# Optimization experiments

Hardware: AMD Instinct MI355X
Metric: run time of the kernel (lower is better)

## Reference

```python
import jax, jax.numpy as jnp
import numpy as np

N_QUBITS = 10
N_LATENT = 6
N_LAYERS = 2
AMP_DIM = 2 ** N_QUBITS  # 1024


def _apply_1q(state, gate, q):
    # state: [B] + [2]*N_QUBITS complex; gate: [2,2]; wire q -> axis q+1 (wire 0 = MSB)
    s = jnp.tensordot(gate, state, axes=[[1], [q + 1]])  # new axis at front
    return jnp.moveaxis(s, 0, q + 1)


def _ry_mat(theta):
    c = jnp.cos(theta / 2)
    s = jnp.sin(theta / 2)
    return jnp.stack([jnp.stack([c, -s]), jnp.stack([s, c])]).astype(jnp.complex64)


def _rz_mat(theta):
    half = theta / 2
    e = jnp.cos(half) + 1j * jnp.sin(half)  # e^{i theta/2}
    zero = jnp.zeros((), jnp.complex64)
    return jnp.stack([jnp.stack([jnp.conj(e), zero]), jnp.stack([zero, e])]).astype(jnp.complex64)


def _cnot(state, c, t):
    # flip target axis where control bit == 1
    ctrl_shape = [1] * (N_QUBITS + 1)
    ctrl_shape[c + 1] = 2
    ctrl = jnp.arange(2).reshape(ctrl_shape)
    return jnp.where(ctrl == 1, jnp.flip(state, axis=t + 1), state)


def _expvals(state):
    # PauliX, PauliY, PauliZ on wires 0..N_LATENT-1  -> [B, 3*N_LATENT]
    rest = tuple(range(1, N_QUBITS))  # axes of the 9 remaining wires after a take
    xs, ys, zs = [], [], []
    for q in range(N_LATENT):
        s0 = jnp.take(state, 0, axis=q + 1)
        s1 = jnp.take(state, 1, axis=q + 1)
        z01 = jnp.conj(s0) * s1
        xs.append(2.0 * jnp.sum(z01.real, axis=rest))
        ys.append(2.0 * jnp.sum(z01.imag, axis=rest))
        zs.append(jnp.sum(jnp.abs(s0) ** 2 - jnp.abs(s1) ** 2, axis=rest))
    return jnp.stack(xs + ys + zs, axis=1)


def _simulate(x, weights):
    B, D = x.shape
    if D < AMP_DIM:
        x = jnp.pad(x, ((0, 0), (0, AMP_DIM - D)))
    else:
        x = x[:, :AMP_DIM]
    norm = jnp.maximum(jnp.linalg.norm(x, axis=-1, keepdims=True), 1e-8)
    x = x / norm
    state = x.astype(jnp.complex64).reshape((B,) + (2,) * N_QUBITS)
    for layer in range(N_LAYERS):
        off = layer * N_QUBITS * 3
        for q in range(N_QUBITS):
            state = _apply_1q(state, _ry_mat(weights[off + q]), q)
        for q in range(N_QUBITS):
            state = _apply_1q(state, _rz_mat(weights[off + N_QUBITS + q]), q)
        for q in range(N_QUBITS):
            state = _cnot(state, q, (q + 1) % N_QUBITS)
        for q in range(N_QUBITS):
            state = _apply_1q(state, _ry_mat(weights[off + 2 * N_QUBITS + q]), q)
    return _expvals(state).astype(jnp.float32)


def setup_inputs() -> dict:
    key = jax.random.key(0)
    k1, k2 = jax.random.split(key)
    B, D = 32768, 768
    x = jax.random.normal(k1, (B, D), dtype=jnp.float32)
    std = np.sqrt(2.0 / (N_QUBITS + N_LAYERS)).astype(np.float32)
    weights = jax.random.normal(k2, (N_LAYERS * N_QUBITS * 3,), dtype=jnp.float32) * std
    return {"x": x, "weights": weights}


def reference(x, weights):
    return _simulate(x, weights)
```

## Files before the change

kernel.cpp:

```cpp
#include <hip/hip_runtime.h>

#define DIN 768

typedef float f2 __attribute__((ext_vector_type(2)));
typedef int i2v __attribute__((ext_vector_type(2)));

#if __has_builtin(__builtin_amdgcn_permlane32_swap)
#define HAVE_PL32 1
#endif
#if __has_builtin(__builtin_amdgcn_permlane16_swap)
#define HAVE_PL16 1
#endif

__device__ __forceinline__ int f2i(float v) { return __builtin_bit_cast(int, v); }
__device__ __forceinline__ float i2f(int v) { return __builtin_bit_cast(float, v); }

template<int CTRL>
__device__ __forceinline__ float dppf(float v) {
  const int i = f2i(v);
  return i2f(__builtin_amdgcn_update_dpp(i, i, CTRL, 0xF, 0xF, true));
}
template<int CTRL>
__device__ __forceinline__ f2 dppf2(f2 v) {
  f2 r; r.x = dppf<CTRL>(v.x); r.y = dppf<CTRL>(v.y); return r;
}

__device__ __forceinline__ f2 wsum2(f2 v) {
  v += dppf2<0xB1>(v);
  v += dppf2<0x4E>(v);
  v += dppf2<0x124>(v);
  v += dppf2<0x128>(v);
#ifdef HAVE_PL16
  { i2v rx = __builtin_amdgcn_permlane16_swap(f2i(v.x), f2i(v.x), false, false);
    i2v ry = __builtin_amdgcn_permlane16_swap(f2i(v.y), f2i(v.y), false, false);
    v.x = i2f(rx.x) + i2f(rx.y);
    v.y = i2f(ry.x) + i2f(ry.y); }
#else
  v.x += __shfl_xor(v.x, 16); v.y += __shfl_xor(v.y, 16);
#endif
#ifdef HAVE_PL32
  { i2v rx = __builtin_amdgcn_permlane32_swap(f2i(v.x), f2i(v.x), false, false);
    i2v ry = __builtin_amdgcn_permlane32_swap(f2i(v.y), f2i(v.y), false, false);
    v.x = i2f(rx.x) + i2f(rx.y);
    v.y = i2f(ry.x) + i2f(ry.y); }
#else
  v.x += __shfl_xor(v.x, 32); v.y += __shfl_xor(v.y, 32);
#endif
  return v;
}

template<int MASK>
__device__ __forceinline__ f2 shflx_f2(f2 v, int lane) {
  f2 r;
  if constexpr (MASK == 1) {
    r = dppf2<0xB1>(v);
  } else if constexpr (MASK == 2) {
    r = dppf2<0x4E>(v);
  } else if constexpr (MASK == 4) {
    r.x = i2f(__builtin_amdgcn_ds_swizzle(f2i(v.x), 0x101F));
    r.y = i2f(__builtin_amdgcn_ds_swizzle(f2i(v.y), 0x101F));
  } else if constexpr (MASK == 8) {
    r = dppf2<0x128>(v);
  } else if constexpr (MASK == 16) {
#ifdef HAVE_PL16
    const i2v a = __builtin_amdgcn_permlane16_swap(f2i(v.x), f2i(v.x), false, false);
    const i2v b = __builtin_amdgcn_permlane16_swap(f2i(v.y), f2i(v.y), false, false);
    const bool hi = (lane >> 4) & 1;
    r.x = hi ? i2f(a.x) : i2f(a.y);
    r.y = hi ? i2f(b.x) : i2f(b.y);
#else
    r.x = __shfl_xor(v.x, 16); r.y = __shfl_xor(v.y, 16);
#endif
  } else if constexpr (MASK == 32) {
#ifdef HAVE_PL32
    const i2v a = __builtin_amdgcn_permlane32_swap(f2i(v.x), f2i(v.x), false, false);
    const i2v b = __builtin_amdgcn_permlane32_swap(f2i(v.y), f2i(v.y), false, false);
    const bool lo = lane < 32;
    r.x = lo ? i2f(a.y) : i2f(a.x);
    r.y = lo ? i2f(b.y) : i2f(b.x);
#else
    r.x = __shfl_xor(v.x, 32); r.y = __shfl_xor(v.y, 32);
#endif
  } else {
    r.x = __shfl_xor(v.x, MASK); r.y = __shfl_xor(v.y, MASK);
  }
  return r;
}

__device__ __forceinline__ int swzf(int i) { return i ^ ((i >> 4) & 31); }

__device__ __forceinline__ int cnotL(int i) {
  const int b9 = (i >> 9) & 1;
  const int b8 = (i >> 8) & 1;
  const int b0 = i & 1;
  return ((i ^ (i >> 1)) & 0xFF) | ((b8 ^ b9 ^ b0) << 8) | ((b9 ^ b0) << 9);
}

template<int RB>
__device__ __forceinline__ void ry1(f2 (&a)[16], float c, float s) {
#pragma unroll
  for (int r = 0; r < 16; ++r) {
    if (!(r & (1 << RB))) {
      const int p = r | (1 << RB);
      const f2 a0 = a[r], a1 = a[p];
      a[r] = a0 * c - a1 * s;
      a[p] = a1 * c + a0 * s;
    }
  }
}
template<int RB>
__device__ __forceinline__ void ry2(f2 (&re)[16], f2 (&im)[16], float c, float s) {
  ry1<RB>(re, c, s);
  ry1<RB>(im, c, s);
}
template<int MASK>
__device__ __forceinline__ void ry1_shfl(int lane, f2 (&a)[16], float c, float s) {
  const float ss = (lane & MASK) ? s : -s;
#pragma unroll
  for (int r = 0; r < 16; ++r) {
    const f2 p = shflx_f2<MASK>(a[r], lane);
    a[r] = a[r] * c + p * ss;
  }
}

template<int RB>
__device__ __forceinline__ void xyr(const f2 (&re)[16], const f2 (&im)[16], f2& aX, f2& aY) {
#pragma unroll
  for (int r = 0; r < 16; ++r) {
    if (!(r & (1 << RB))) {
      const int p = r | (1 << RB);
      aX += re[r] * re[p] + im[r] * im[p];
      aY += re[r] * im[p] - im[r] * re[p];
    }
  }
}
template<int MASK>
__device__ __forceinline__ void xys(int lane, const f2 (&re)[16], const f2 (&im)[16], f2& aX, f2& aY) {
  const float sgn = (lane & MASK) ? -1.f : 1.f;
#pragma unroll
  for (int r = 0; r < 16; ++r) {
    const f2 pr = shflx_f2<MASK>(re[r], lane);
    const f2 pi = shflx_f2<MASK>(im[r], lane);
    aX += re[r] * pr + im[r] * pi;
    aY += (re[r] * pi - im[r] * pr) * sgn;
  }
}

__global__ void qae_prep(const float* __restrict__ w, float2* __restrict__ ws) {
  const int i = threadIdx.x;
  if (i < 50) {
    float s, c; __sincosf(0.5f * w[i], &s, &c);
    ws[i] = make_float2(c, s);
  } else if (i < 56) {
    float s, c; __sincosf(w[i], &s, &c);
    ws[i] = make_float2(c, s);
  } else if (i < 60) {
    ws[i] = make_float2(1.f, 0.f);
  } else if (i < 70) {
    const int q = i - 60;
    float s, c; __sincosf(0.5f * (w[20 + q] + w[30 + q]), &s, &c);
    ws[i] = make_float2(c, s);
  }
  if (i < 16) {
    float p1 = 0.f, p2 = 0.f;
#pragma unroll
    for (int k = 0; k < 4; ++k) {
      const float sg = ((i >> k) & 1) ? 0.5f : -0.5f;
      p1 += sg * w[10 + 3 - k];
      p2 += sg * w[40 + 3 - k];
    }
    float s, c;
    __sincosf(p1, &s, &c); ws[70 + i] = make_float2(c, s);
    __sincosf(p2, &s, &c); ws[86 + i] = make_float2(c, s);
  }
  if (i < 64) {
    float p1 = 0.f, p2 = 0.f;
#pragma unroll
    for (int b = 0; b < 6; ++b) {
      const float sg = ((i >> b) & 1) ? 0.5f : -0.5f;
      p1 += sg * w[10 + 9 - b];
      p2 += sg * w[40 + 9 - b];
    }
    float s, c;
    __sincosf(p1, &s, &c); ws[102 + i] = make_float2(c, s);
    __sincosf(p2, &s, &c); ws[166 + i] = make_float2(c, s);
  }
}

#define STC8(boff) (*reinterpret_cast<f2*>(reinterpret_cast<char*>(stc) + (boff)))

__global__ __launch_bounds__(64) void qae_main(const float* __restrict__ x,
                                               const float2* __restrict__ gt,
                                               float* __restrict__ out, int Btot) {
  __shared__ f2 stc[1024];
  const int lane = threadIdx.x;
  const int b0   = blockIdx.x * 2, b1 = b0 + 1;
  const bool has1 = (b1 < Btot);

  const float2 L1 = gt[102 + lane];
  const float2 L2 = gt[166 + lane];

  const int bA8   = swzf(lane << 4) << 3;
  const int sL8   = swzf(lane) << 3;
  const int bCA8  = swzf(cnotL(lane << 4)) << 3;
  const int bCB8  = swzf(cnotL(lane)) << 3;

  f2 g[16];
  f2 ss = (f2){0.f, 0.f};
  const float* x0 = x + (size_t)b0 * DIN;
  const float* x1 = x + (size_t)b1 * DIN;
#pragma unroll
  for (int r = 0; r < 12; ++r) {
    const int i = (r << 6) | lane;
    const float va = x0[i];
    const float vb = has1 ? x1[i] : 0.f;
    g[r] = (f2){va, vb};
    ss += g[r] * g[r];
  }
#pragma unroll
  for (int r = 12; r < 16; ++r) g[r] = (f2){0.f, 0.f};
  ss = wsum2(ss);
  const f2 inv = (f2){1.f / fmaxf(ss.x, 1e-16f), 1.f / fmaxf(ss.y, 1e-16f)};

  float2 cs;
  cs = gt[0]; ry1<3>(g, cs.x, cs.y);
  cs = gt[1]; ry1<2>(g, cs.x, cs.y);
  cs = gt[2]; ry1<1>(g, cs.x, cs.y);
  cs = gt[3]; ry1<0>(g, cs.x, cs.y);
  cs = gt[4]; ry1_shfl<32>(lane, g, cs.x, cs.y);
  cs = gt[5]; ry1_shfl<16>(lane, g, cs.x, cs.y);
  cs = gt[6]; ry1_shfl<8>(lane, g, cs.x, cs.y);
  cs = gt[7]; ry1_shfl<4>(lane, g, cs.x, cs.y);
  cs = gt[8]; ry1_shfl<2>(lane, g, cs.x, cs.y);
  cs = gt[9]; ry1_shfl<1>(lane, g, cs.x, cs.y);

  f2 re[16], im[16];
#pragma unroll
  for (int r = 0; r < 16; ++r) {
    const float2 R = gt[70 + r];
    const float kre = R.x * L1.x - R.y * L1.y;
    const float kim = R.x * L1.y + R.y * L1.x;
    re[r] = g[r] * kre;
    im[r] = g[r] * kim;
  }

#pragma unroll
  for (int r = 0; r < 16; ++r) STC8((swzf(r << 6) << 3) ^ sL8) = re[r];
#pragma unroll
  for (int r = 0; r < 16; ++r) re[r] = STC8(bCA8 ^ (swzf(cnotL(r)) << 3));
#pragma unroll
  for (int r = 0; r < 16; ++r) STC8((swzf(r << 6) << 3) ^ sL8) = im[r];
#pragma unroll
  for (int r = 0; r < 16; ++r) im[r] = STC8(bCA8 ^ (swzf(cnotL(r)) << 3));

  cs = gt[66]; ry2<3>(re, im, cs.x, cs.y);
  cs = gt[67]; ry2<2>(re, im, cs.x, cs.y);
  cs = gt[68]; ry2<1>(re, im, cs.x, cs.y);
  cs = gt[69]; ry2<0>(re, im, cs.x, cs.y);
  cs = gt[64]; ry1_shfl<2>(lane, re, cs.x, cs.y); ry1_shfl<2>(lane, im, cs.x, cs.y);
  cs = gt[65]; ry1_shfl<1>(lane, re, cs.x, cs.y); ry1_shfl<1>(lane, im, cs.x, cs.y);

#pragma unroll
  for (int r = 0; r < 16; ++r) STC8(bA8 ^ (r << 3)) = re[r];
#pragma unroll
  for (int r = 0; r < 16; ++r) re[r] = STC8((swzf(r << 6) << 3) ^ sL8);
#pragma unroll
  for (int r = 0; r < 16; ++r) STC8(bA8 ^ (r << 3)) = im[r];
#pragma unroll
  for (int r = 0; r < 16; ++r) im[r] = STC8((swzf(r << 6) << 3) ^ sL8);

  cs = gt[60]; ry2<3>(re, im, cs.x, cs.y);
  cs = gt[61]; ry2<2>(re, im, cs.x, cs.y);
  cs = gt[62]; ry2<1>(re, im, cs.x, cs.y);
  cs = gt[63]; ry2<0>(re, im, cs.x, cs.y);

#pragma unroll
  for (int r = 0; r < 16; ++r) {
    const float2 R = gt[86 + r];
    const float kre = R.x * L2.x - R.y * L2.y;
    const float kim = R.x * L2.y + R.y * L2.x;
    const f2 nre = re[r] * kre - im[r] * kim;
    im[r] = re[r] * kim + im[r] * kre;
    re[r] = nre;
  }

#pragma unroll
  for (int r = 0; r < 16; ++r) STC8((swzf(r << 6) << 3) ^ sL8) = re[r];
#pragma unroll
  for (int r = 0; r < 16; ++r) re[r] = STC8(bCB8 ^ (swzf(cnotL(r << 6)) << 3));
#pragma unroll
  for (int r = 0; r < 16; ++r) STC8((swzf(r << 6) << 3) ^ sL8) = im[r];
#pragma unroll
  for (int r = 0; r < 16; ++r) im[r] = STC8(bCB8 ^ (swzf(cnotL(r << 6)) << 3));

  f2 a18[18];
#pragma unroll
  for (int k = 0; k < 12; ++k) a18[k] = (f2){0.f, 0.f};

  {
    f2 psum = (f2){0.f, 0.f};
    f2 z0 = (f2){0.f,0.f}, z1 = (f2){0.f,0.f}, z2 = (f2){0.f,0.f}, z3 = (f2){0.f,0.f};
#pragma unroll
    for (int r = 0; r < 16; ++r) {
      const f2 p = re[r] * re[r] + im[r] * im[r];
      psum += p;
      z0 += (r & 8) ? -p : p;
      z1 += (r & 4) ? -p : p;
      z2 += (r & 2) ? -p : p;
      z3 += (r & 1) ? -p : p;
    }
    a18[12] = z0; a18[13] = z1; a18[14] = z2; a18[15] = z3;
    a18[16] = ((lane >> 5) & 1) ? -psum : psum;
    a18[17] = ((lane >> 4) & 1) ? -psum : psum;
  }

  xyr<3>(re, im, a18[0], a18[6]);
  xyr<2>(re, im, a18[1], a18[7]);
  xyr<1>(re, im, a18[2], a18[8]);
  xyr<0>(re, im, a18[3], a18[9]);
  xys<32>(lane, re, im, a18[4], a18[10]);
  xys<16>(lane, re, im, a18[5], a18[11]);

#pragma unroll
  for (int k = 0; k < 18; ++k) {
    f2 v = a18[k];
    v += dppf2<0xB1>(v);
    v += dppf2<0x4E>(v);
    a18[k] = v;
  }
  float* red = reinterpret_cast<float*>(stc);
  if ((lane & 3) == 0) {
    const int q = lane >> 2;
    f2* redf2 = reinterpret_cast<f2*>(red);
#pragma unroll
    for (int k = 0; k < 18; ++k) redf2[q * 20 + k] = a18[k];
  }
  if (lane < 36) {
    const int c  = (lane >= 18) ? 1 : 0;
    const int j  = lane - 18 * c;
    const int jq = (j < 6) ? j : ((j < 12) ? j - 6 : j - 12);
    const int jp = (j < 6) ? (j + 12) : ((j >= 12) ? (j - 12) : j);
    float S = 0.f, P = 0.f;
#pragma unroll
    for (int q = 0; q < 16; ++q) {
      S += red[(q * 20 + j ) * 2 + c];
      P += red[(q * 20 + jp) * 2 + c];
    }
    const float fac  = (jq < 4) ? 2.f : 1.f;
    const float2 fa  = gt[50 + jq];
    const float invc = c ? inv.y : inv.x;
    float o;
    if (j < 6)       o = (fac * S * fa.x + P * fa.y) * invc;
    else if (j < 12) o = fac * S * invc;
    else             o = (S * fa.x - fac * P * fa.y) * invc;
    if (c == 0 || has1) out[(size_t)(b0 + c) * 18 + j] = o;
  }
}

extern "C" void kernel_launch(void* const* d_in, const int* in_sizes, int n_in,
                              void* d_out, int out_size, void* d_ws, size_t ws_size,
                              hipStream_t stream) {
  const float* x = (const float*)d_in[0];
  const float* w = (const float*)d_in[1];
  float* out = (float*)d_out;
  float2* ws = (float2*)d_ws;
  const int B = in_sizes[0] / DIN;
  qae_prep<<<dim3(1), dim3(1024), 0, stream>>>(w, ws);
  const int grid = (B + 1) / 2;
  qae_main<<<dim3(grid), dim3(64), 0, stream>>>(x, (const float2*)ws, out, B);
}
```

Baseline: 102.9 us.

## Load input with float4 in lane-contiguous layout and transpose via LDS

Input rows are now loaded as float4 with each lane owning 16 contiguous amplitudes, so the low six qubits are in registers and only two need cross-lane shuffles. After applying those gates, the state is transposed through shared memory into the original lane-strided layout for the remaining four RY gates. This replaces four expensive cross-lane shuffles (masks 4, 8, 16, 32) with an extra LDS round trip. It also changes coalescing: per-lane 16-byte loads instead of scalar strided loads.

```diff
diff --git a/kernel.cpp b/kernel.cpp
--- a/kernel.cpp
+++ b/kernel.cpp
@@ -56,11 +56,6 @@
     r = dppf2<0xB1>(v);
   } else if constexpr (MASK == 2) {
     r = dppf2<0x4E>(v);
-  } else if constexpr (MASK == 4) {
-    r.x = i2f(__builtin_amdgcn_ds_swizzle(f2i(v.x), 0x101F));
-    r.y = i2f(__builtin_amdgcn_ds_swizzle(f2i(v.y), 0x101F));
-  } else if constexpr (MASK == 8) {
-    r = dppf2<0x128>(v);
   } else if constexpr (MASK == 16) {
 #ifdef HAVE_PL16
     const i2v a = __builtin_amdgcn_permlane16_swap(f2i(v.x), f2i(v.x), false, false);
@@ -210,29 +205,39 @@
   const float* x0 = x + (size_t)b0 * DIN;
   const float* x1 = x + (size_t)b1 * DIN;
 #pragma unroll
-  for (int r = 0; r < 12; ++r) {
-    const int i = (r << 6) | lane;
-    const float va = x0[i];
-    const float vb = has1 ? x1[i] : 0.f;
-    g[r] = (f2){va, vb};
-    ss += g[r] * g[r];
-  }
-#pragma unroll
-  for (int r = 12; r < 16; ++r) g[r] = (f2){0.f, 0.f};
+  for (int t = 0; t < 4; ++t) {
+    const int idx = lane * 16 + 4 * t;
+    float4 va = make_float4(0.f, 0.f, 0.f, 0.f);
+    float4 vb = make_float4(0.f, 0.f, 0.f, 0.f);
+    if (idx < DIN) {
+      va = *reinterpret_cast<const float4*>(x0 + idx);
+      if (has1) vb = *reinterpret_cast<const float4*>(x1 + idx);
+    }
+    g[4*t+0] = (f2){va.x, vb.x}; g[4*t+1] = (f2){va.y, vb.y};
+    g[4*t+2] = (f2){va.z, vb.z}; g[4*t+3] = (f2){va.w, vb.w};
+#pragma unroll
+    for (int k = 0; k < 4; ++k) ss += g[4*t+k] * g[4*t+k];
+  }
   ss = wsum2(ss);
   const f2 inv = (f2){1.f / fmaxf(ss.x, 1e-16f), 1.f / fmaxf(ss.y, 1e-16f)};
 
   float2 cs;
+  cs = gt[6]; ry1<3>(g, cs.x, cs.y);
+  cs = gt[7]; ry1<2>(g, cs.x, cs.y);
+  cs = gt[8]; ry1<1>(g, cs.x, cs.y);
+  cs = gt[9]; ry1<0>(g, cs.x, cs.y);
+  cs = gt[4]; ry1_shfl<2>(lane, g, cs.x, cs.y);
+  cs = gt[5]; ry1_shfl<1>(lane, g, cs.x, cs.y);
+
+#pragma unroll
+  for (int r = 0; r < 16; ++r) STC8(bA8 ^ (r << 3)) = g[r];
+#pragma unroll
+  for (int r = 0; r < 16; ++r) g[r] = STC8((swzf(r << 6) << 3) ^ sL8);
+
   cs = gt[0]; ry1<3>(g, cs.x, cs.y);
   cs = gt[1]; ry1<2>(g, cs.x, cs.y);
   cs = gt[2]; ry1<1>(g, cs.x, cs.y);
   cs = gt[3]; ry1<0>(g, cs.x, cs.y);
-  cs = gt[4]; ry1_shfl<32>(lane, g, cs.x, cs.y);
-  cs = gt[5]; ry1_shfl<16>(lane, g, cs.x, cs.y);
-  cs = gt[6]; ry1_shfl<8>(lane, g, cs.x, cs.y);
-  cs = gt[7]; ry1_shfl<4>(lane, g, cs.x, cs.y);
-  cs = gt[8]; ry1_shfl<2>(lane, g, cs.x, cs.y);
-  cs = gt[9]; ry1_shfl<1>(lane, g, cs.x, cs.y);
 
   f2 re[16], im[16];
 #pragma unroll
```

New measurement: 103.2 us. About the same (+0.2%).
